# Kernel optimization log

Hardware: AMD Instinct MI355X
Metric: run time of the kernel (lower is better)

## Reference

```python
import jax, jax.numpy as jnp
import numpy as np

N_NODES = 100000
N_EDGES = 3200000
F_IN = 4
HID = 32
N_ROUNDS = 17  # proj_in + 16 hidden conv layers


def setup_inputs() -> dict:
    key = jax.random.key(0)
    ks = jax.random.split(key, 8)
    x = jax.random.normal(ks[0], (N_NODES, F_IN), dtype=jnp.float32)
    edge_index = jax.random.randint(ks[1], (2, N_EDGES), 0, N_NODES, dtype=jnp.int64)
    s = 0.2
    # Linear weights stored as [in, out] (torch stores [out, in]; math y = x @ W_in_out)
    A_in = jax.random.normal(ks[2], (F_IN, HID), dtype=jnp.float32) * s
    B_in = jax.random.normal(ks[3], (F_IN, HID), dtype=jnp.float32) * s
    A_conv = jax.random.normal(ks[4], (N_ROUNDS - 1, HID, HID), dtype=jnp.float32) * s
    B_conv = jax.random.normal(ks[5], (N_ROUNDS - 1, HID, HID), dtype=jnp.float32) * s
    W_out = jax.random.normal(ks[6], (HID, 1), dtype=jnp.float32) * s
    b_out = jax.random.normal(ks[7], (1,), dtype=jnp.float32) * s
    return {"x": x, "edge_index": edge_index, "A_in": A_in, "B_in": B_in,
            "A_conv": A_conv, "B_conv": B_conv, "W_out": W_out, "b_out": b_out}


def _masking_conv(x, src, dst, inv_deg, Wa, Wb):
    # scatter-mean of neighbor (source) features onto destination nodes
    msg_sum = jax.ops.segment_sum(x[src], dst, num_segments=N_NODES)  # [N, d]
    avg_msg = msg_sum * inv_deg  # mean aggregation; isolated nodes -> 0
    h = avg_msg @ Wa + x @ Wb
    # nn.Softmax() on a 2-D tensor resolves to dim=1 (per-node over features)
    return jax.nn.softmax(h, axis=1)


def reference(x, edge_index, A_in, B_in, A_conv, B_conv, W_out, b_out):
    src, dst = edge_index[0], edge_index[1]
    deg = jax.ops.segment_sum(jnp.ones((N_EDGES,), jnp.float32), dst,
                              num_segments=N_NODES)
    inv_deg = (1.0 / jnp.maximum(deg, 1.0))[:, None]  # [N, 1]

    h = _masking_conv(x, src, dst, inv_deg, A_in, B_in)  # proj_in: inner softmax only

    def step(h, w):
        Wa, Wb = w
        h = _masking_conv(h, src, dst, inv_deg, Wa, Wb)
        return jax.nn.softmax(h, axis=0), None  # outer softmax over nodes

    h, _ = jax.lax.scan(step, h, (A_conv, B_conv))
    out = jax.nn.softmax(h @ W_out + b_out, axis=0)  # [N, 1]
    return out
```

## Files before the change

kernel.cpp:

```cpp
#include <hip/hip_runtime.h>

#define NGF 256
#define NBMAX 2048
#define CSTR 64

typedef float    f2 __attribute__((ext_vector_type(2)));
typedef float    f4 __attribute__((ext_vector_type(4)));
typedef float    f8 __attribute__((ext_vector_type(8)));
typedef _Float16 h8 __attribute__((ext_vector_type(8)));

__device__ __forceinline__ unsigned f2key(float x){
  unsigned b = __float_as_uint(x);
  return (b & 0x80000000u) ? ~b : (b | 0x80000000u);
}
__device__ __forceinline__ float key2f(unsigned k){
  return (k & 0x80000000u) ? __uint_as_float(k ^ 0x80000000u) : __uint_as_float(~k);
}

__device__ __forceinline__ f4 dec4(unsigned w){
  f2 a = __builtin_amdgcn_cvt_pk_f32_fp8((int)w, false);
  f2 b = __builtin_amdgcn_cvt_pk_f32_fp8((int)w, true);
  f4 r; r[0]=a[0]; r[1]=a[1]; r[2]=b[0]; r[3]=b[1];
  return r;
}
__device__ __forceinline__ f8 dec8(uint2 w){
  f4 lo = dec4(w.x), hi = dec4(w.y);
  f8 r;
  r[0]=lo[0]; r[1]=lo[1]; r[2]=lo[2]; r[3]=lo[3];
  r[4]=hi[0]; r[5]=hi[1]; r[6]=hi[2]; r[7]=hi[3];
  return r;
}



__global__ __launch_bounds__(256) void k_bucketA(const int* __restrict__ ei,
    int* __restrict__ bucket, int* __restrict__ lbasemat,
    int E, int n, int span, unsigned magic){
  __shared__ int lcnt[NGF];
  __shared__ int lbase[NGF+1];
  __shared__ int sStage[2048];
  __shared__ int sScan[256];
  int tid = threadIdx.x;
  lcnt[tid] = 0;
  __syncthreads();
  int base = blockIdx.x*2048;
  int val[8], meta[8];
  #pragma unroll
  for (int i=0;i<8;i++){
    int e = base + i*256 + tid;
    meta[i] = -1;
    val[i] = 0;
    if (e < E){
      int d = ei[E + e];
      int s = ei[e];
      if ((unsigned)d < (unsigned)n && (unsigned)s < (unsigned)n){
        int gf = (int)__umulhi((unsigned)d, magic);
        int dl = d - gf*span;
        val[i] = (dl << 17) | s;
        int rank = atomicAdd(&lcnt[gf], 1);
        meta[i] = (gf << 11) | rank;
      }
    }
  }
  __syncthreads();
  int v = lcnt[tid];
  sScan[tid] = v;
  __syncthreads();
  for (int o=1;o<256;o<<=1){
    int t = (tid>=o) ? sScan[tid-o] : 0;
    __syncthreads();
    if (tid>=o) sScan[tid] += t;
    __syncthreads();
  }
  lbase[tid] = sScan[tid] - v;
  if (tid == 255) lbase[NGF] = sScan[255];
  __syncthreads();
  #pragma unroll
  for (int i=0;i<8;i++){
    if (meta[i] >= 0){
      int gf   = meta[i] >> 11;
      int rank = meta[i] & 0x7FF;
      sStage[lbase[gf] + rank] = val[i];
    }
  }
  int* row = lbasemat + (size_t)blockIdx.x*(NGF+1);
  row[tid] = lbase[tid];
  if (tid == 0) row[NGF] = lbase[NGF];
  __syncthreads();
  int* bp = bucket + (size_t)blockIdx.x*2048;
  #pragma unroll
  for (int i=0;i<2;i++){
    int idx = i*256 + tid;
    ((int4*)bp)[idx] = ((const int4*)sStage)[idx];
  }
}

__global__ __launch_bounds__(256) void k_rtot(const int* __restrict__ lbasemat,
                                              int* __restrict__ rt, int nb){
  __shared__ int red[256];
  int gf = blockIdx.x, tid = threadIdx.x;
  int s = 0;
  for (int b=tid; b<nb; b+=256){
    const int* row = lbasemat + (size_t)b*(NGF+1) + gf;
    s += row[1] - row[0];
  }
  red[tid] = s;
  __syncthreads();
  for (int o=128;o>0;o>>=1){
    if (tid < o) red[tid] += red[tid+o];
    __syncthreads();
  }
  if (tid == 0) rt[gf] = red[0];
}

__global__ void k_rscan(const int* __restrict__ rt, int* __restrict__ rbase,
                        int* __restrict__ offsN){
  __shared__ int sc[256];
  int tid = threadIdx.x;
  int v = rt[tid];
  sc[tid] = v;
  __syncthreads();
  for (int o=1;o<256;o<<=1){
    int t = (tid>=o) ? sc[tid-o] : 0;
    __syncthreads();
    if (tid>=o) sc[tid] += t;
    __syncthreads();
  }
  rbase[tid] = sc[tid] - v;
  if (tid == 255){ rbase[NGF] = sc[255]; offsN[0] = sc[255]; }
}

__global__ __launch_bounds__(256) void k_fill3(const int* __restrict__ bucket,
    const int* __restrict__ lbasemat, const int* __restrict__ rbase,
    int* __restrict__ csr, int* __restrict__ offs, float* __restrict__ invdeg,
    int n, int span, int nb){
  __shared__ int sLo[NBMAX];
  __shared__ int sPre[NBMAX+1];
  __shared__ int sScan[256];
  __shared__ int sHist[512];
  __shared__ int sCur[512];
  int gf = blockIdx.x, tid = threadIdx.x;
  for (int b=tid; b<nb; b+=256){
    const int* row = lbasemat + (size_t)b*(NGF+1) + gf;
    int lo = row[0], hi = row[1];
    sLo[b]  = b*2048 + lo;
    sPre[b] = hi - lo;
  }
  for (int t=tid; t<512; t+=256){ sHist[t] = 0; }
  __syncthreads();
  int C = (nb + 255) >> 8;
  int st = tid*C, en = st + C; if (en > nb) en = nb; if (st > nb) st = nb;
  int a0 = 0;
  for (int i=st;i<en;i++) a0 += sPre[i];
  sScan[tid] = a0;
  __syncthreads();
  for (int o=1;o<256;o<<=1){
    int t = (tid>=o) ? sScan[tid-o] : 0;
    __syncthreads();
    if (tid>=o) sScan[tid] += t;
    __syncthreads();
  }
  int ex = sScan[tid] - a0;
  int run = ex;
  for (int i=st;i<en;i++){ int t = sPre[i]; sPre[i] = run; run += t; }
  if (tid == 255) sPre[nb] = sScan[255];
  __syncthreads();
  int total = sPre[nb];
  int rb = rbase[gf];
  for (int i=tid; i<total; i+=256){
    int lo = 0, hi = nb;
    while (hi - lo > 1){ int mid = (lo+hi) >> 1; if (sPre[mid] <= i) lo = mid; else hi = mid; }
    int v = bucket[sLo[lo] + (i - sPre[lo])];
    atomicAdd(&sHist[v >> 17], 1);
  }
  __syncthreads();
  int C2 = (span + 255) >> 8;
  int st2 = tid*C2, en2 = st2 + C2; if (en2 > span) en2 = span; if (st2 > span) st2 = span;
  int a2 = 0;
  for (int i=st2;i<en2;i++) a2 += sHist[i];
  sScan[tid] = a2;
  __syncthreads();
  for (int o=1;o<256;o<<=1){
    int t = (tid>=o) ? sScan[tid-o] : 0;
    __syncthreads();
    if (tid>=o) sScan[tid] += t;
    __syncthreads();
  }
  int ex2 = sScan[tid] - a2;
  int run2 = ex2;
  for (int i=st2;i<en2;i++){ sCur[i] = run2; run2 += sHist[i]; }
  __syncthreads();
  for (int t=tid; t<span; t+=256){
    int node = gf*span + t;
    if (node < n){
      int deg = sHist[t];
      offs[node]   = rb + sCur[t];
      invdeg[node] = (deg > 0) ? 1.0f/(float)deg : 0.0f;
    }
  }
  __syncthreads();
  for (int i=tid; i<total; i+=256){
    int lo = 0, hi = nb;
    while (hi - lo > 1){ int mid = (lo+hi) >> 1; if (sPre[mid] <= i) lo = mid; else hi = mid; }
    int v  = bucket[sLo[lo] + (i - sPre[lo])];
    int dl = v >> 17;
    int sc = v & 0x1FFFF;
    int pos = atomicAdd(&sCur[dl], 1);
    csr[rb + pos] = sc;
  }
}


__global__ __launch_bounds__(256) void k_in(const float* __restrict__ x, unsigned char* __restrict__ uout,
    const int* __restrict__ offs, const int* __restrict__ csr, const float* __restrict__ invdeg,
    const float* __restrict__ A, const float* __restrict__ B, int n){
  __shared__ float sA[128], sB[128];
  int tid = threadIdx.x;
  if (tid < 128){ sA[tid]=A[tid]; sB[tid]=B[tid]; }
  __syncthreads();
  int node = blockIdx.x*256 + tid;
  if (node >= n) return;
  float4 s = {0,0,0,0};
  int b0=offs[node], e0=offs[node+1];
  for (int k=b0;k<e0;k++){
    int sid = csr[k];
    float4 v = ((const float4*)x)[sid];
    s.x+=v.x; s.y+=v.y; s.z+=v.z; s.w+=v.w;
  }
  float idg = invdeg[node];
  s.x*=idg; s.y*=idg; s.z*=idg; s.w*=idg;
  float4 xr = ((const float4*)x)[node];
  float z[32];
  #pragma unroll
  for (int j=0;j<32;j++){
    z[j] = s.x*sA[j] + s.y*sA[32+j] + s.z*sA[64+j] + s.w*sA[96+j]
         + xr.x*sB[j] + xr.y*sB[32+j] + xr.z*sB[64+j] + xr.w*sB[96+j];
  }
  float m = z[0];
  #pragma unroll
  for (int j=1;j<32;j++) m = fmaxf(m,z[j]);
  float sum=0.0f;
  #pragma unroll
  for (int j=0;j<32;j++){ z[j]=expf(z[j]-m); sum+=z[j]; }
  float r = 1.0f/sum;
  unsigned pk[8];
  #pragma unroll
  for (int q=0;q<8;q++){
    int w0 = __builtin_amdgcn_cvt_pk_fp8_f32(z[4*q]*r,   z[4*q+1]*r, 0,  false);
    w0     = __builtin_amdgcn_cvt_pk_fp8_f32(z[4*q+2]*r, z[4*q+3]*r, w0, true);
    pk[q] = (unsigned)w0;
  }
  uint4* op = (uint4*)(uout + (size_t)node*32);
  op[0] = make_uint4(pk[0],pk[1],pk[2],pk[3]);
  op[1] = make_uint4(pk[4],pk[5],pk[6],pk[7]);
}


__global__ __launch_bounds__(256) void k_conv(
    const unsigned char* __restrict__ uin, unsigned char* __restrict__ uout,
    const int* __restrict__ offs, const int* __restrict__ csr,
    const float* __restrict__ invdeg,
    const float* __restrict__ Wa, const float* __restrict__ Wb,
    const float* __restrict__ cs_prev, float Rscale, float base,
    float* __restrict__ cs_next, int n){
  __shared__ float sWa[1024], sWb[1024];
  __shared__ float sCol[32];
  __shared__ unsigned char sU[64][32];
  int tid = threadIdx.x;
  float rcf = 1.0f;
  if (cs_prev) rcf = 131072.0f / ((float)n + cs_prev[(tid>>3)*CSTR]);
  ((f4*)sWa)[tid] = ((const f4*)Wa)[tid] * rcf;
  ((f4*)sWb)[tid] = ((const f4*)Wb)[tid] * rcf;
  if (tid < 32) sCol[tid] = 0.0f;
  __syncthreads();

  int lane = tid & 63;
  int wv   = tid >> 6;
  int q    = lane >> 4;
  int c    = lane & 15;
  int tile = blockIdx.x*64 + wv*16;
  int node = tile + c;
  bool gv = node < n;

  h8 waLo, waHi, wbLo, wbHi;
  #pragma unroll
  for (int j=0;j<8;j++){
    int k = q*8 + j;
    waLo[j] = (_Float16)sWa[k*32 + c];
    waHi[j] = (_Float16)sWa[k*32 + c + 16];
    wbLo[j] = (_Float16)sWb[k*32 + c];
    wbHi[j] = (_Float16)sWb[k*32 + c + 16];
  }

  f8 a0 = {0,0,0,0,0,0,0,0}, a1 = {0,0,0,0,0,0,0,0};
  f8 a2 = {0,0,0,0,0,0,0,0}, a3 = {0,0,0,0,0,0,0,0};
  int b0 = gv ? offs[node]   : 0;
  int e0 = gv ? offs[node+1] : 0;
  const uint2* ub = (const uint2*)uin;
  int k = b0;
  for (; k+8<=e0; k+=8){
    int s0=csr[k],   s1=csr[k+1], s2=csr[k+2], s3=csr[k+3];
    int s4=csr[k+4], s5=csr[k+5], s6=csr[k+6], s7=csr[k+7];
    uint2 v0 = ub[(size_t)s0*4 + q];
    uint2 v1 = ub[(size_t)s1*4 + q];
    uint2 v2 = ub[(size_t)s2*4 + q];
    uint2 v3 = ub[(size_t)s3*4 + q];
    uint2 v4 = ub[(size_t)s4*4 + q];
    uint2 v5 = ub[(size_t)s5*4 + q];
    uint2 v6 = ub[(size_t)s6*4 + q];
    uint2 v7 = ub[(size_t)s7*4 + q];
    a0 += dec8(v0); a1 += dec8(v1); a2 += dec8(v2); a3 += dec8(v3);
    a0 += dec8(v4); a1 += dec8(v5); a2 += dec8(v6); a3 += dec8(v7);
  }
  for (; k<e0; k++) a0 += dec8(ub[(size_t)csr[k]*4 + q]);
  a0 = (a0 + a1) + (a2 + a3);
  float idg = gv ? invdeg[node] : 0.0f;
  float bavg = (idg != 0.0f) ? base : 0.0f;
  a0 = a0*idg + bavg;
  h8 afrag = __builtin_convertvector(a0, h8);
  f8 od = {0,0,0,0,0,0,0,0};
  if (gv) od = dec8(ub[(size_t)node*4 + q]) + base;
  h8 ofrag = __builtin_convertvector(od, h8);

  f4 z1 = {0,0,0,0}, z2 = {0,0,0,0};
  z1 = __builtin_amdgcn_mfma_f32_16x16x32_f16(ofrag, wbLo, z1, 0, 0, 0);
  z1 = __builtin_amdgcn_mfma_f32_16x16x32_f16(afrag, waLo, z1, 0, 0, 0);
  z2 = __builtin_amdgcn_mfma_f32_16x16x32_f16(ofrag, wbHi, z2, 0, 0, 0);
  z2 = __builtin_amdgcn_mfma_f32_16x16x32_f16(afrag, waHi, z2, 0, 0, 0);
  z1 *= Rscale; z2 *= Rscale;

  f4 mx, sm;
  #pragma unroll
  for (int r=0;r<4;r++) mx[r] = fmaxf(z1[r], z2[r]);
  #pragma unroll
  for (int s=1;s<16;s<<=1){
    #pragma unroll
    for (int r=0;r<4;r++) mx[r] = fmaxf(mx[r], __shfl_xor(mx[r], s));
  }
  #pragma unroll
  for (int r=0;r<4;r++){
    z1[r] = expf(z1[r]-mx[r]);
    z2[r] = expf(z2[r]-mx[r]);
    sm[r] = z1[r] + z2[r];
  }
  #pragma unroll
  for (int s=1;s<16;s<<=1){
    #pragma unroll
    for (int r=0;r<4;r++) sm[r] += __shfl_xor(sm[r], s);
  }
  float cs1 = 0.0f, cs2 = 0.0f;
  #pragma unroll
  for (int r=0;r<4;r++){
    float rs = 1.0f/sm[r];
    float v1 = expf(z1[r]*rs) - 1.0f;
    float v2 = expf(z2[r]*rs) - 1.0f;
    int p1 = __builtin_amdgcn_cvt_pk_fp8_f32(v1, v1, 0, false);
    int p2 = __builtin_amdgcn_cvt_pk_fp8_f32(v2, v2, 0, false);
    f2 d1 = __builtin_amdgcn_cvt_pk_f32_fp8(p1, false);
    f2 d2 = __builtin_amdgcn_cvt_pk_f32_fp8(p2, false);
    int lrow = wv*16 + q*4 + r;
    sU[lrow][c]      = (unsigned char)(p1 & 0xff);
    sU[lrow][c + 16] = (unsigned char)(p2 & 0xff);
    if (tile + q*4 + r < n){
      cs1 += d1[0];
      cs2 += d2[0];
    }
  }
  cs1 += __shfl_xor(cs1, 16); cs1 += __shfl_xor(cs1, 32);
  cs2 += __shfl_xor(cs2, 16); cs2 += __shfl_xor(cs2, 32);
  if (lane < 16){
    atomicAdd(&sCol[c],      cs1);
    atomicAdd(&sCol[c + 16], cs2);
  }
  __syncthreads();
  if (tid < 32) atomicAdd(&cs_next[tid*CSTR], sCol[tid]);
  int row = tid >> 2;
  int jj  = tid & 3;
  int gnode = blockIdx.x*64 + row;
  if (gnode < n){
    uint2 val = *(const uint2*)&sU[row][jj*8];
    *(uint2*)(uout + (size_t)gnode*32 + jj*8) = val;
  }
}


__global__ __launch_bounds__(256) void k_out1(const unsigned char* __restrict__ u, const float* __restrict__ W,
    const float* __restrict__ bptr, const float* __restrict__ cs_last,
    float* __restrict__ z, unsigned* __restrict__ zmaxkey, int n){
  __shared__ float ws[32];
  __shared__ float red[256];
  int tid = threadIdx.x;
  if (tid < 32) ws[tid] = W[tid] * (1.0f / ((float)n + cs_last[tid*CSTR]));
  __syncthreads();
  float sws = 0.0f;
  #pragma unroll
  for (int j=0;j<32;j++) sws += ws[j];
  int node = blockIdx.x*256 + tid;
  float zz = -3.0e38f;
  if (node < n){
    float acc = bptr[0] + sws;
    const uint4* ur = (const uint4*)(u + (size_t)node*32);
    uint4 w0 = ur[0], w1 = ur[1];
    unsigned wd[8] = {w0.x,w0.y,w0.z,w0.w,w1.x,w1.y,w1.z,w1.w};
    #pragma unroll
    for (int q=0;q<8;q++){
      f4 a = dec4(wd[q]);
      f4 w = ((const f4*)ws)[q];
      acc += a[0]*w[0] + a[1]*w[1] + a[2]*w[2] + a[3]*w[3];
    }
    z[node]=acc; zz=acc;
  }
  red[tid]=zz; __syncthreads();
  for (int s=128;s>0;s>>=1){
    if (tid<s) red[tid]=fmaxf(red[tid],red[tid+s]);
    __syncthreads();
  }
  if (tid==0) atomicMax(zmaxkey, f2key(red[0]));
}

__global__ __launch_bounds__(256) void k_out2(const float* __restrict__ z, const unsigned* __restrict__ zmaxkey,
                                              float* __restrict__ zsum, int n){
  __shared__ float red[256];
  int tid = threadIdx.x;
  int node = blockIdx.x*256 + tid;
  float zmax = key2f(*zmaxkey);
  float v = (node<n) ? expf(z[node]-zmax) : 0.0f;
  red[tid]=v; __syncthreads();
  for (int s=128;s>0;s>>=1){
    if (tid<s) red[tid]+=red[tid+s];
    __syncthreads();
  }
  if (tid==0) atomicAdd(zsum, red[0]);
}

__global__ __launch_bounds__(256) void k_out3(const float* __restrict__ z, const unsigned* __restrict__ zmaxkey,
                                              const float* __restrict__ zsum, float* __restrict__ out, int n){
  int node = blockIdx.x*256 + threadIdx.x;
  if (node < n){
    float zmax = key2f(*zmaxkey);
    out[node] = expf(z[node]-zmax) / (*zsum);
  }
}


extern "C" void kernel_launch(void* const* d_in, const int* in_sizes, int n_in,
                              void* d_out, int out_size, void* d_ws, size_t ws_size,
                              hipStream_t stream) {
  const float* x      = (const float*)d_in[0];
  const int*   ei     = (const int*)d_in[1];
  const float* A_in   = (const float*)d_in[2];
  const float* B_in   = (const float*)d_in[3];
  const float* A_conv = (const float*)d_in[4];
  const float* B_conv = (const float*)d_in[5];
  const float* W_out  = (const float*)d_in[6];
  const float* b_out  = (const float*)d_in[7];
  const int N = in_sizes[0] / 4;
  const int E = in_sizes[1] / 2;
  const int NROUNDS = 16;

  char* w = (char*)d_ws;
  size_t o = 0;
  auto alloc = [&](size_t bytes)->char* {
    char* p = w + o;
    o = (o + bytes + 15) & ~(size_t)15;
    return p;
  };
  float*    colsum  = (float*)   alloc((size_t)NROUNDS*32*CSTR*4);
  unsigned* zmaxkey = (unsigned*)alloc(4);
  float*    zsum    = (float*)   alloc(4);
  size_t ctrl_bytes = o;
  int    nb      = (E + 2047) / 2048;
  int    span    = (N + NGF - 1) / NGF;
  int*   offs    = (int*)  alloc((size_t)(N+1)*4);
  float* invdeg  = (float*)alloc((size_t)N*4);
  int*   csr     = (int*)  alloc((size_t)E*4);
  int*   bucket  = (int*)  alloc((size_t)nb*2048*4);
  int*   lbasemat= (int*)  alloc((size_t)nb*(NGF+1)*4);
  int*   rt      = (int*)  alloc((size_t)NGF*4);
  int*   rbase   = (int*)  alloc((size_t)(NGF+1)*4);
  unsigned char* uA = (unsigned char*)alloc((size_t)N*32);
  unsigned char* uB = (unsigned char*)alloc((size_t)N*32);
  float* zbuf    = (float*)alloc((size_t)N*4);
  (void)ws_size; (void)n_in; (void)out_size;

  hipMemsetAsync(d_ws, 0, ctrl_bytes, stream);

  unsigned magic = (unsigned)((((unsigned long long)1 << 32) + (unsigned long long)span - 1)
                              / (unsigned long long)span);
  int gridN = (N + 255) / 256;
  int gridC = (N + 63) / 64;

  k_bucketA<<<nb, 256, 0, stream>>>(ei, bucket, lbasemat, E, N, span, magic);
  k_rtot   <<<NGF, 256, 0, stream>>>(lbasemat, rt, nb);
  k_rscan  <<<1, 256, 0, stream>>>(rt, rbase, offs + N);
  k_fill3  <<<NGF, 256, 0, stream>>>(bucket, lbasemat, rbase, csr, offs, invdeg, N, span, nb);

  k_in<<<gridN, 256, 0, stream>>>(x, uA, offs, csr, invdeg, A_in, B_in, N);

  const float R17 = 1.0f/131072.0f;
  for (int r = 0; r < NROUNDS; r++){
    const float* Wa = A_conv + (size_t)r*32*32;
    const float* Wb = B_conv + (size_t)r*32*32;
    const float* cs_prev = (r == 0) ? nullptr : (colsum + (size_t)(r-1)*32*CSTR);
    float*       cs_next = colsum + (size_t)r*32*CSTR;
    float        Rs      = (r == 0) ? 1.0f : R17;
    float        base    = (r == 0) ? 0.0f : 1.0f;
    const unsigned char* ui = (r & 1) ? uB : uA;
    unsigned char*       uo = (r & 1) ? uA : uB;
    k_conv<<<gridC, 256, 0, stream>>>(ui, uo, offs, csr, invdeg, Wa, Wb, cs_prev, Rs, base, cs_next, N);
  }

  k_out1<<<gridN, 256, 0, stream>>>(uA, W_out, b_out, colsum + (size_t)(NROUNDS-1)*32*CSTR, zbuf, zmaxkey, N);
  k_out2<<<gridN, 256, 0, stream>>>(zbuf, zmaxkey, zsum, N);
  k_out3<<<gridN, 256, 0, stream>>>(zbuf, zmaxkey, zsum, (float*)d_out, N);
}
```

Before: 1.006 ms.

## Enlarge edge bucket blocks, transpose bucket offsets, simplify CSR fill loop

Each bucketing block now handles 8192 edges instead of 2048, which cuts the number of buckets per group by a factor of four. The per-block offset matrix is transposed so that the per-group reduction and fill kernels read it contiguously. The fill kernel drops its prefix scan and per-element binary search, and each thread now walks whole bucket segments directly. The cost is an extra transpose kernel, more register pressure in bucketA, and worse load balance, because segment lengths differ between threads.

```diff
diff --git a/kernel.cpp b/kernel.cpp
--- a/kernel.cpp
+++ b/kernel.cpp
@@ -1,7 +1,8 @@
 #include <hip/hip_runtime.h>
 
 #define NGF 256
-#define NBMAX 2048
+#define BAE 8192
+#define BAVPT 32
 #define CSTR 64
 
 typedef float    f2 __attribute__((ext_vector_type(2)));
@@ -32,21 +33,20 @@
 }
 
 
-
 __global__ __launch_bounds__(256) void k_bucketA(const int* __restrict__ ei,
     int* __restrict__ bucket, int* __restrict__ lbasemat,
     int E, int n, int span, unsigned magic){
   __shared__ int lcnt[NGF];
   __shared__ int lbase[NGF+1];
-  __shared__ int sStage[2048];
+  __shared__ int sStage[BAE];
   __shared__ int sScan[256];
   int tid = threadIdx.x;
   lcnt[tid] = 0;
   __syncthreads();
-  int base = blockIdx.x*2048;
-  int val[8], meta[8];
-  #pragma unroll
-  for (int i=0;i<8;i++){
+  int base = blockIdx.x*BAE;
+  int val[BAVPT], meta[BAVPT];
+  #pragma unroll
+  for (int i=0;i<BAVPT;i++){
     int e = base + i*256 + tid;
     meta[i] = -1;
     val[i] = 0;
@@ -58,7 +58,7 @@
         int dl = d - gf*span;
         val[i] = (dl << 17) | s;
         int rank = atomicAdd(&lcnt[gf], 1);
-        meta[i] = (gf << 11) | rank;
+        meta[i] = (gf << 13) | rank;
       }
     }
   }
@@ -76,10 +76,10 @@
   if (tid == 255) lbase[NGF] = sScan[255];
   __syncthreads();
   #pragma unroll
-  for (int i=0;i<8;i++){
+  for (int i=0;i<BAVPT;i++){
     if (meta[i] >= 0){
-      int gf   = meta[i] >> 11;
-      int rank = meta[i] & 0x7FF;
+      int gf   = meta[i] >> 13;
+      int rank = meta[i] & 0x1FFF;
       sStage[lbase[gf] + rank] = val[i];
     }
   }
@@ -87,23 +87,36 @@
   row[tid] = lbase[tid];
   if (tid == 0) row[NGF] = lbase[NGF];
   __syncthreads();
-  int* bp = bucket + (size_t)blockIdx.x*2048;
-  #pragma unroll
-  for (int i=0;i<2;i++){
+  int* bp = bucket + (size_t)blockIdx.x*BAE;
+  #pragma unroll
+  for (int i=0;i<BAE/1024;i++){
     int idx = i*256 + tid;
     ((int4*)bp)[idx] = ((const int4*)sStage)[idx];
   }
 }
 
-__global__ __launch_bounds__(256) void k_rtot(const int* __restrict__ lbasemat,
-                                              int* __restrict__ rt, int nb){
+__global__ __launch_bounds__(1024) void k_transp(const int* __restrict__ in,
+    int* __restrict__ out, int nb, int nbp){
+  __shared__ int t[32][33];
+  int bx = blockIdx.x*32, by = blockIdx.y*32;
+  int tx = threadIdx.x, ty = threadIdx.y;
+  int b = bx + ty;
+  int g = by + tx;
+  if (b < nb && g < NGF+1) t[ty][tx] = in[(size_t)b*(NGF+1) + g];
+  __syncthreads();
+  int g2 = by + ty;
+  int b2 = bx + tx;
+  if (g2 < NGF+1 && b2 < nb) out[(size_t)g2*nbp + b2] = t[tx][ty];
+}
+
+__global__ __launch_bounds__(256) void k_rtot(const int* __restrict__ lbT,
+                                              int* __restrict__ rt, int nb, int nbp){
   __shared__ int red[256];
   int gf = blockIdx.x, tid = threadIdx.x;
+  const int* lo = lbT + (size_t)gf*nbp;
+  const int* hi = lo + nbp;
   int s = 0;
-  for (int b=tid; b<nb; b+=256){
-    const int* row = lbasemat + (size_t)b*(NGF+1) + gf;
-    s += row[1] - row[0];
-  }
+  for (int b=tid; b<nb; b+=256) s += hi[b] - lo[b];
   red[tid] = s;
   __syncthreads();
   for (int o=128;o>0;o>>=1){
@@ -130,48 +143,24 @@
   if (tid == 255){ rbase[NGF] = sc[255]; offsN[0] = sc[255]; }
 }
 
-__global__ __launch_bounds__(256) void k_fill3(const int* __restrict__ bucket,
-    const int* __restrict__ lbasemat, const int* __restrict__ rbase,
+__global__ __launch_bounds__(256) void k_fill4(const int* __restrict__ bucket,
+    const int* __restrict__ lbT, const int* __restrict__ rbase,
     int* __restrict__ csr, int* __restrict__ offs, float* __restrict__ invdeg,
-    int n, int span, int nb){
-  __shared__ int sLo[NBMAX];
-  __shared__ int sPre[NBMAX+1];
-  __shared__ int sScan[256];
+    int n, int span, int nb, int nbp){
   __shared__ int sHist[512];
   __shared__ int sCur[512];
+  __shared__ int sScan[256];
   int gf = blockIdx.x, tid = threadIdx.x;
+  int rb = rbase[gf];
+  const int* rowLo = lbT + (size_t)gf*nbp;
+  const int* rowHi = rowLo + nbp;
+  for (int i=tid; i<512; i+=256) sHist[i] = 0;
+  __syncthreads();
   for (int b=tid; b<nb; b+=256){
-    const int* row = lbasemat + (size_t)b*(NGF+1) + gf;
-    int lo = row[0], hi = row[1];
-    sLo[b]  = b*2048 + lo;
-    sPre[b] = hi - lo;
-  }
-  for (int t=tid; t<512; t+=256){ sHist[t] = 0; }
-  __syncthreads();
-  int C = (nb + 255) >> 8;
-  int st = tid*C, en = st + C; if (en > nb) en = nb; if (st > nb) st = nb;
-  int a0 = 0;
-  for (int i=st;i<en;i++) a0 += sPre[i];
-  sScan[tid] = a0;
-  __syncthreads();
-  for (int o=1;o<256;o<<=1){
-    int t = (tid>=o) ? sScan[tid-o] : 0;
-    __syncthreads();
-    if (tid>=o) sScan[tid] += t;
-    __syncthreads();
-  }
-  int ex = sScan[tid] - a0;
-  int run = ex;
-  for (int i=st;i<en;i++){ int t = sPre[i]; sPre[i] = run; run += t; }
-  if (tid == 255) sPre[nb] = sScan[255];
-  __syncthreads();
-  int total = sPre[nb];
-  int rb = rbase[gf];
-  for (int i=tid; i<total; i+=256){
-    int lo = 0, hi = nb;
-    while (hi - lo > 1){ int mid = (lo+hi) >> 1; if (sPre[mid] <= i) lo = mid; else hi = mid; }
-    int v = bucket[sLo[lo] + (i - sPre[lo])];
-    atomicAdd(&sHist[v >> 17], 1);
+    int lo = rowLo[b], hi = rowHi[b];
+    const int* bp = bucket + (size_t)b*BAE;
+    for (int i=lo; i<hi; i++)
+      atomicAdd(&sHist[((unsigned)bp[i]) >> 17], 1);
   }
   __syncthreads();
   int C2 = (span + 255) >> 8;
@@ -199,14 +188,14 @@
     }
   }
   __syncthreads();
-  for (int i=tid; i<total; i+=256){
-    int lo = 0, hi = nb;
-    while (hi - lo > 1){ int mid = (lo+hi) >> 1; if (sPre[mid] <= i) lo = mid; else hi = mid; }
-    int v  = bucket[sLo[lo] + (i - sPre[lo])];
-    int dl = v >> 17;
-    int sc = v & 0x1FFFF;
-    int pos = atomicAdd(&sCur[dl], 1);
-    csr[rb + pos] = sc;
+  for (int b=tid; b<nb; b+=256){
+    int lo = rowLo[b], hi = rowHi[b];
+    const int* bp = bucket + (size_t)b*BAE;
+    for (int i=lo; i<hi; i++){
+      int v = bp[i];
+      int pos = atomicAdd(&sCur[((unsigned)v) >> 17], 1);
+      csr[rb + pos] = v & 0x1FFFF;
+    }
   }
 }
 
@@ -469,13 +458,14 @@
   unsigned* zmaxkey = (unsigned*)alloc(4);
   float*    zsum    = (float*)   alloc(4);
   size_t ctrl_bytes = o;
-  int    nb      = (E + 2047) / 2048;
+  int    nb      = (E + BAE-1) / BAE;
   int    span    = (N + NGF - 1) / NGF;
   int*   offs    = (int*)  alloc((size_t)(N+1)*4);
   float* invdeg  = (float*)alloc((size_t)N*4);
   int*   csr     = (int*)  alloc((size_t)E*4);
-  int*   bucket  = (int*)  alloc((size_t)nb*2048*4);
+  int*   bucket  = (int*)  alloc((size_t)nb*BAE*4);
   int*   lbasemat= (int*)  alloc((size_t)nb*(NGF+1)*4);
+  int*   lbT     = (int*)  alloc((size_t)(NGF+1)*nb*4);
   int*   rt      = (int*)  alloc((size_t)NGF*4);
   int*   rbase   = (int*)  alloc((size_t)(NGF+1)*4);
   unsigned char* uA = (unsigned char*)alloc((size_t)N*32);
@@ -491,9 +481,14 @@
   int gridC = (N + 63) / 64;
 
   k_bucketA<<<nb, 256, 0, stream>>>(ei, bucket, lbasemat, E, N, span, magic);
-  k_rtot   <<<NGF, 256, 0, stream>>>(lbasemat, rt, nb);
-  k_rscan  <<<1, 256, 0, stream>>>(rt, rbase, offs + N);
-  k_fill3  <<<NGF, 256, 0, stream>>>(bucket, lbasemat, rbase, csr, offs, invdeg, N, span, nb);
+  {
+    dim3 tb(32,32);
+    dim3 tg((nb + 31)/32, (NGF+1 + 31)/32);
+    k_transp<<<tg, tb, 0, stream>>>(lbasemat, lbT, nb, nb);
+  }
+  k_rtot <<<NGF, 256, 0, stream>>>(lbT, rt, nb, nb);
+  k_rscan<<<1, 256, 0, stream>>>(rt, rbase, offs + N);
+  k_fill4<<<NGF, 256, 0, stream>>>(bucket, lbT, rbase, csr, offs, invdeg, N, span, nb, nb);
 
   k_in<<<gridN, 256, 0, stream>>>(x, uA, offs, csr, invdeg, A_in, B_in, N);
 
```

New measurement: 955.8 us. 5.0% less time.
